# Kernel tuning notes

Measured on AMD Instinct MI355X. Metric: run time of the kernel, lower is better.

## Reference

```python
import jax, jax.numpy as jnp
import numpy as np

N_NODES = 100000
N_EDGES = 1600000
IN_CH = 128
HID = 128
BN_EPS = 1e-5


def setup_inputs() -> dict:
    key = jax.random.key(0)
    ks = jax.random.split(key, 16)
    x = jax.random.normal(ks[0], (N_NODES, IN_CH), dtype=jnp.float32)
    edge_index = jax.random.randint(ks[1], (2, N_EDGES), 0, N_NODES, dtype=jnp.int32)
    edge_attr = jax.random.uniform(ks[2], (N_EDGES,), dtype=jnp.float32)
    def glorot(k, fan_in, fan_out):
        s = jnp.sqrt(6.0 / (fan_in + fan_out))
        return jax.random.uniform(k, (fan_in, fan_out), dtype=jnp.float32, minval=-s, maxval=s)
    W1 = glorot(ks[3], IN_CH, HID)
    b1 = jnp.zeros((HID,), jnp.float32)
    gamma1 = jnp.ones((HID,), jnp.float32)
    beta1 = jnp.zeros((HID,), jnp.float32)
    W2 = glorot(ks[4], HID, HID)
    b2 = jnp.zeros((HID,), jnp.float32)
    gamma2 = jnp.ones((HID,), jnp.float32)
    beta2 = jnp.zeros((HID,), jnp.float32)
    W3 = glorot(ks[5], HID, 1)
    b3 = jnp.zeros((1,), jnp.float32)
    return {"x": x, "edge_index": edge_index, "edge_attr": edge_attr,
            "W1": W1, "b1": b1, "gamma1": gamma1, "beta1": beta1,
            "W2": W2, "b2": b2, "gamma2": gamma2, "beta2": beta2,
            "W3": W3, "b3": b3}


def _gcn_norm(edge_index, edge_weight, num_nodes):
    # PyG gcn_norm with add_self_loops=True, self-loop weight 1.0
    sl = jnp.arange(num_nodes, dtype=edge_index.dtype)
    row = jnp.concatenate([edge_index[0], sl])  # source
    col = jnp.concatenate([edge_index[1], sl])  # target
    w = jnp.concatenate([edge_weight, jnp.ones((num_nodes,), edge_weight.dtype)])
    deg = jax.ops.segment_sum(w, col, num_segments=num_nodes)
    dinv = jnp.where(deg > 0, jax.lax.rsqrt(jnp.maximum(deg, 1e-30)), 0.0)
    norm = dinv[row] * w * dinv[col]
    return row, col, norm


def _gcn_conv(x, W, b, row, col, norm, num_nodes):
    xw = x @ W                       # [N, out]
    msg = xw[row] * norm[:, None]    # gather + scale, [E+N, out]
    out = jax.ops.segment_sum(msg, col, num_segments=num_nodes)  # scatter-add
    return out + b


def _batchnorm(x, gamma, beta):
    mean = jnp.mean(x, axis=0)
    var = jnp.mean(jnp.square(x - mean), axis=0)  # biased var (torch BN)
    return (x - mean) * jax.lax.rsqrt(var + BN_EPS) * gamma + beta


def reference(x, edge_index, edge_attr, W1, b1, gamma1, beta1, W2, b2, gamma2, beta2, W3, b3):
    n = x.shape[0]
    row, col, norm = _gcn_norm(edge_index, edge_attr, n)
    h = _gcn_conv(x, W1, b1, row, col, norm, n)
    h = jax.nn.relu(_batchnorm(h, gamma1, beta1))  # dropout = identity (eval)
    h = _gcn_conv(h, W2, b2, row, col, norm, n)
    h = jax.nn.relu(_batchnorm(h, gamma2, beta2))
    out = _gcn_conv(h, W3, b3, row, col, norm, n)  # [N, 1]
    return out
```

## Files before the change

kernel.cpp:

```cpp
#include <hip/hip_runtime.h>
#include <hip/hip_bf16.h>


#define HID 128
#define BN_EPS 1e-5f
#define BK 64

typedef __attribute__((ext_vector_type(8))) short bf16x8;
typedef __attribute__((ext_vector_type(4))) float f32x4;

static inline size_t alignup(size_t x){ return (x + 255) & ~(size_t)255; }


__global__ void k_initcur(int* cursor, int n){
  int i = blockIdx.x*256 + threadIdx.x;
  if (i < n) cursor[i] = 0;
}

__global__ void k_fill_direct(const int* __restrict__ ei, const float* __restrict__ attr,
                              int* __restrict__ cursor, int2* __restrict__ csr, int E){
  int e = blockIdx.x*256 + threadIdx.x;
  if (e >= E) return;
  int src = ei[e];
  int dst = ei[E + e];
  int pos = atomicAdd(&cursor[dst], 1);
  if (pos < BK)
    csr[(size_t)dst*BK + pos] = make_int2(src, __float_as_int(attr[e]));
}

__global__ __launch_bounds__(256) void k_degdinv(const int2* __restrict__ csr,
    const int* __restrict__ cursor, float* __restrict__ dinv, int N){
  int node = blockIdx.x*32 + (threadIdx.x >> 3);
  int l = threadIdx.x & 7;
  if (node >= N) return;
  int m = min(cursor[node], BK);
  float s = 0.f;
  for (int j = l; j < m; j += 8)
    s += __int_as_float(csr[(size_t)node*BK + j].y);
  s += __shfl_xor(s, 1, 8);
  s += __shfl_xor(s, 2, 8);
  s += __shfl_xor(s, 4, 8);
  if (l == 0) dinv[node] = 1.0f / sqrtf(1.0f + s);
}

__global__ __launch_bounds__(256) void k_wfin(int2* __restrict__ csr,
    const int* __restrict__ cursor, const float* __restrict__ dinv, int N){
  int node = blockIdx.x*32 + (threadIdx.x >> 3);
  int l = threadIdx.x & 7;
  if (node >= N) return;
  int m = min(cursor[node], BK);
  float di = dinv[node];
  for (int j = l; j < m; j += 8){
    int2 t = csr[(size_t)node*BK + j];
    float w = dinv[t.x] * __int_as_float(t.y) * di;
    csr[(size_t)node*BK + j] = make_int2(t.x, __float_as_int(w));
  }
}


static __device__ inline float2 bf16pair(unsigned int u){
  __hip_bfloat162 h = *(__hip_bfloat162*)&u;
  return __bfloat1622float2(h);
}

static __device__ inline unsigned int packpair(float x, float y){
  __hip_bfloat162 p = __float22bfloat162_rn({x, y});
  return *(unsigned int*)&p;
}

static __device__ inline uint2 pack_bf16x4(float4 a){
  uint2 r;
  r.x = packpair(a.x, a.y);
  r.y = packpair(a.z, a.w);
  return r;
}

static __device__ inline unsigned short bfbits(float v){
  __hip_bfloat16 h = __float2bfloat16(v);
  return *(unsigned short*)&h;
}

__global__ void k_wtprep(const float* __restrict__ Wg, unsigned short* __restrict__ WTg){
  int idx = blockIdx.x*256 + threadIdx.x;
  int k   = idx >> 7;
  int col = idx & 127;
  WTg[(size_t)col*128 + k] = bfbits(Wg[(size_t)k*128 + col]);
}

template<bool BN, bool AB16>
__device__ inline void gemm_body(const void* __restrict__ Av,
    const unsigned short* __restrict__ WTg, const float* __restrict__ coef,
    unsigned int* __restrict__ C, int n, int bid){
  int lane = threadIdx.x & 63;
  int wv4  = threadIdx.x >> 6;
  int l16  = lane & 15;
  int kg   = lane >> 4;
  int row_base = bid*128 + wv4*32;
  int nm1 = n - 1;
  int a0row = min(row_base + l16,      nm1);
  int a1row = min(row_base + 16 + l16, nm1);

  f32x4 acc[2][8] = {};
  #pragma unroll
  for (int k0 = 0; k0 < 128; k0 += 32){
    int k = k0 + kg*8;
    float4 sca, scb, sha, shb;
    if (BN){
      sca = *(const float4*)(coef + k);
      scb = *(const float4*)(coef + k + 4);
      sha = *(const float4*)(coef + 128 + k);
      shb = *(const float4*)(coef + 128 + k + 4);
    }
    bf16x8 a0, a1;
    if constexpr (AB16){
      const unsigned int* A = (const unsigned int*)Av;
      uint4 u0 = *(const uint4*)(A + (size_t)a0row*64 + (k >> 1));
      uint4 u1 = *(const uint4*)(A + (size_t)a1row*64 + (k >> 1));
      #pragma unroll
      for (int half = 0; half < 2; ++half){
        uint4 u = half ? u1 : u0;
        float2 p0 = bf16pair(u.x), p1 = bf16pair(u.y);
        float2 p2 = bf16pair(u.z), p3 = bf16pair(u.w);
        if (BN){
          p0.x = fmaxf(fmaf(p0.x, sca.x, sha.x), 0.f);
          p0.y = fmaxf(fmaf(p0.y, sca.y, sha.y), 0.f);
          p1.x = fmaxf(fmaf(p1.x, sca.z, sha.z), 0.f);
          p1.y = fmaxf(fmaf(p1.y, sca.w, sha.w), 0.f);
          p2.x = fmaxf(fmaf(p2.x, scb.x, shb.x), 0.f);
          p2.y = fmaxf(fmaf(p2.y, scb.y, shb.y), 0.f);
          p3.x = fmaxf(fmaf(p3.x, scb.z, shb.z), 0.f);
          p3.y = fmaxf(fmaf(p3.y, scb.w, shb.w), 0.f);
        }
        union { bf16x8 v; unsigned int u[4]; } c;
        c.u[0] = packpair(p0.x, p0.y);
        c.u[1] = packpair(p1.x, p1.y);
        c.u[2] = packpair(p2.x, p2.y);
        c.u[3] = packpair(p3.x, p3.y);
        if (half) a1 = c.v; else a0 = c.v;
      }
    } else {
      const float* A = (const float*)Av;
      float4 lo0 = *(const float4*)(A + (size_t)a0row*HID + k);
      float4 hi0 = *(const float4*)(A + (size_t)a0row*HID + k + 4);
      float4 lo1 = *(const float4*)(A + (size_t)a1row*HID + k);
      float4 hi1 = *(const float4*)(A + (size_t)a1row*HID + k + 4);
      union { bf16x8 v; uint2 u[2]; } a0c, a1c;
      a0c.u[0] = pack_bf16x4(lo0); a0c.u[1] = pack_bf16x4(hi0);
      a1c.u[0] = pack_bf16x4(lo1); a1c.u[1] = pack_bf16x4(hi1);
      a0 = a0c.v; a1 = a1c.v;
    }
    #pragma unroll
    for (int ct = 0; ct < 8; ++ct){
      int col = ct*16 + l16;
      bf16x8 b = *(const bf16x8*)(WTg + (size_t)col*128 + k);
      acc[0][ct] = __builtin_amdgcn_mfma_f32_16x16x32_bf16(a0, b, acc[0][ct], 0,0,0);
      acc[1][ct] = __builtin_amdgcn_mfma_f32_16x16x32_bf16(a1, b, acc[1][ct], 0,0,0);
    }
  }

  #pragma unroll
  for (int rt = 0; rt < 2; ++rt){
    int growb = row_base + rt*16 + kg*4;
    #pragma unroll
    for (int ct = 0; ct < 8; ++ct){
      #pragma unroll
      for (int r = 0; r < 4; ++r){
        float v = acc[rt][ct][r];
        float o = __shfl_xor(v, 1);
        if (!(lane & 1)){
          int grow = growb + r;
          if (grow < n){
            C[(size_t)grow*64 + ct*8 + (l16 >> 1)] = packpair(v, o);
          }
        }
      }
    }
  }
}

__global__ __launch_bounds__(256) void k_gemm_mfma(const float* __restrict__ A,
    const unsigned short* __restrict__ WTg,
    unsigned int* __restrict__ C, int n){
  gemm_body<false,false>(A, WTg, nullptr, C, n, blockIdx.x);
}

__global__ __launch_bounds__(256) void k_gemm_mfma_bn16(const unsigned int* __restrict__ A,
    const unsigned short* __restrict__ WTg, const float* __restrict__ coef,
    unsigned int* __restrict__ C, int n){
  gemm_body<true,true>(A, WTg, coef, C, n, blockIdx.x);
}


struct Acc8 { float a0,a1,a2,a3,a4,a5,a6,a7; };

static __device__ inline void fma8(Acc8& a, uint4 v, float wt){
  float2 p0 = bf16pair(v.x), p1 = bf16pair(v.y);
  float2 p2 = bf16pair(v.z), p3 = bf16pair(v.w);
  a.a0 = fmaf(wt, p0.x, a.a0); a.a1 = fmaf(wt, p0.y, a.a1);
  a.a2 = fmaf(wt, p1.x, a.a2); a.a3 = fmaf(wt, p1.y, a.a3);
  a.a4 = fmaf(wt, p2.x, a.a4); a.a5 = fmaf(wt, p2.y, a.a5);
  a.a6 = fmaf(wt, p3.x, a.a6); a.a7 = fmaf(wt, p3.y, a.a7);
}

__global__ __launch_bounds__(256) void k_gather128(const unsigned int* __restrict__ xwb,
    const int2* __restrict__ csr, const int* __restrict__ cursor,
    const float* __restrict__ dinv, const float* __restrict__ bias,
    unsigned int* __restrict__ out, int n){
  int node = blockIdx.x*4 + (threadIdx.x >> 6);
  int lane = threadIdx.x & 63;
  if (node >= n) return;
  int l16 = lane & 15;
  int eg  = lane >> 4;
  size_t base = (size_t)node*BK;
  int m = min(cursor[node], BK);
  Acc8 a = {0,0,0,0,0,0,0,0};
  if (eg == 0){
    float di = dinv[node];
    float sw = di * di;
    uint4 sv = *(const uint4*)(xwb + (size_t)node*64 + l16*4);
    float4 b0 = *(const float4*)(bias + l16*8);
    float4 b1 = *(const float4*)(bias + l16*8 + 4);
    a.a0 = b0.x; a.a1 = b0.y; a.a2 = b0.z; a.a3 = b0.w;
    a.a4 = b1.x; a.a5 = b1.y; a.a6 = b1.z; a.a7 = b1.w;
    fma8(a, sv, sw);
  }
  int j = eg;
  for (; j + 12 < m; j += 16){
    int2 e0 = csr[base + j];
    int2 e1 = csr[base + j + 4];
    int2 e2 = csr[base + j + 8];
    int2 e3 = csr[base + j + 12];
    uint4 v0 = *(const uint4*)(xwb + (size_t)e0.x*64 + l16*4);
    uint4 v1 = *(const uint4*)(xwb + (size_t)e1.x*64 + l16*4);
    uint4 v2 = *(const uint4*)(xwb + (size_t)e2.x*64 + l16*4);
    uint4 v3 = *(const uint4*)(xwb + (size_t)e3.x*64 + l16*4);
    fma8(a, v0, __int_as_float(e0.y));
    fma8(a, v1, __int_as_float(e1.y));
    fma8(a, v2, __int_as_float(e2.y));
    fma8(a, v3, __int_as_float(e3.y));
  }
  for (; j < m; j += 4){
    int2 ea = csr[base + j];
    uint4 va = *(const uint4*)(xwb + (size_t)ea.x*64 + l16*4);
    fma8(a, va, __int_as_float(ea.y));
  }
  a.a0 += __shfl_xor(a.a0, 16); a.a1 += __shfl_xor(a.a1, 16);
  a.a2 += __shfl_xor(a.a2, 16); a.a3 += __shfl_xor(a.a3, 16);
  a.a4 += __shfl_xor(a.a4, 16); a.a5 += __shfl_xor(a.a5, 16);
  a.a6 += __shfl_xor(a.a6, 16); a.a7 += __shfl_xor(a.a7, 16);
  a.a0 += __shfl_xor(a.a0, 32); a.a1 += __shfl_xor(a.a1, 32);
  a.a2 += __shfl_xor(a.a2, 32); a.a3 += __shfl_xor(a.a3, 32);
  a.a4 += __shfl_xor(a.a4, 32); a.a5 += __shfl_xor(a.a5, 32);
  a.a6 += __shfl_xor(a.a6, 32); a.a7 += __shfl_xor(a.a7, 32);
  if (eg == 0){
    uint4 r;
    r.x = packpair(a.a0, a.a1);
    r.y = packpair(a.a2, a.a3);
    r.z = packpair(a.a4, a.a5);
    r.w = packpair(a.a6, a.a7);
    *(uint4*)(out + (size_t)node*64 + l16*4) = r;
  }
}

__global__ __launch_bounds__(256) void k_bnstats(const unsigned int* __restrict__ h,
                                                 float* stats, int n){
  __shared__ float ls0[256], ls1[256], lq0[256], lq1[256];
  int p  = threadIdx.x & 63;
  int r0 = blockIdx.x*4 + (threadIdx.x >> 6);
  float s0=0.f, s1=0.f, q0=0.f, q1=0.f;
  for (int r = r0; r < n; r += gridDim.x*4){
    float2 v = bf16pair(h[(size_t)r*64 + p]);
    s0 += v.x; q0 = fmaf(v.x, v.x, q0);
    s1 += v.y; q1 = fmaf(v.y, v.y, q1);
  }
  ls0[threadIdx.x]=s0; ls1[threadIdx.x]=s1; lq0[threadIdx.x]=q0; lq1[threadIdx.x]=q1;
  __syncthreads();
  if (threadIdx.x < 64){
    int t = threadIdx.x;
    s0 = ls0[t]+ls0[t+64]+ls0[t+128]+ls0[t+192];
    s1 = ls1[t]+ls1[t+64]+ls1[t+128]+ls1[t+192];
    q0 = lq0[t]+lq0[t+64]+lq0[t+128]+lq0[t+192];
    q1 = lq1[t]+lq1[t+64]+lq1[t+128]+lq1[t+192];
    atomicAdd(&stats[2*t],       s0);
    atomicAdd(&stats[2*t+1],     s1);
    atomicAdd(&stats[128+2*t],   q0);
    atomicAdd(&stats[128+2*t+1], q1);
  }
}

__global__ void k_bnfin(const float* __restrict__ stats, const float* __restrict__ gamma,
                        const float* __restrict__ beta, float* coef, int n){
  int c = threadIdx.x;
  float inv_n = 1.0f / (float)n;
  float mean = stats[c] * inv_n;
  float var = fmaxf(stats[128 + c] * inv_n - mean*mean, 0.f);
  float sc = gamma[c] / sqrtf(var + BN_EPS);
  coef[c] = sc;
  coef[128 + c] = fmaf(-mean, sc, beta[c]);
}

__global__ __launch_bounds__(256) void k_dotW3(const unsigned int* __restrict__ h,
    const float* __restrict__ coef, const float* __restrict__ W3,
    float* __restrict__ xw3, int n){
  int lane = threadIdx.x & 31;
  int row = blockIdx.x*8 + (threadIdx.x >> 5);
  if (row >= n) return;
  uint2 u = *(const uint2*)(h + (size_t)row*64 + lane*2);
  float2 va = bf16pair(u.x), vb = bf16pair(u.y);
  float4 sc = *(const float4*)(coef + lane*4);
  float4 sh = *(const float4*)(coef + 128 + lane*4);
  float4 w  = *(const float4*)(W3 + lane*4);
  float acc = fmaxf(fmaf(va.x, sc.x, sh.x), 0.f) * w.x
            + fmaxf(fmaf(va.y, sc.y, sh.y), 0.f) * w.y
            + fmaxf(fmaf(vb.x, sc.z, sh.z), 0.f) * w.z
            + fmaxf(fmaf(vb.y, sc.w, sh.w), 0.f) * w.w;
  #pragma unroll
  for (int mm = 1; mm < 32; mm <<= 1) acc += __shfl_xor(acc, mm, 32);
  if (lane == 0) xw3[row] = acc;
}

__global__ void k_gather1(const float* __restrict__ xw3, const int2* __restrict__ csr,
    const int* __restrict__ cursor, const float* __restrict__ dinv,
    const float* __restrict__ b3, float* __restrict__ out, int n){
  int i = blockIdx.x*256 + threadIdx.x;
  if (i >= n) return;
  float di = dinv[i];
  float acc = fmaf(di*di, xw3[i], b3[0]);
  size_t base = (size_t)i*BK;
  int m = min(cursor[i], BK);
  for (int j = 0; j < m; ++j){
    int2 e = csr[base + j];
    acc = fmaf(__int_as_float(e.y), xw3[e.x], acc);
  }
  out[i] = acc;
}

extern "C" void kernel_launch(void* const* d_in, const int* in_sizes, int n_in,
                              void* d_out, int out_size, void* d_ws, size_t ws_size,
                              hipStream_t stream){
  const float* x    = (const float*)d_in[0];
  const int*   ei   = (const int*)  d_in[1];
  const float* attr = (const float*)d_in[2];
  const float* W1   = (const float*)d_in[3];
  const float* b1   = (const float*)d_in[4];
  const float* g1   = (const float*)d_in[5];
  const float* be1  = (const float*)d_in[6];
  const float* W2   = (const float*)d_in[7];
  const float* b2   = (const float*)d_in[8];
  const float* g2   = (const float*)d_in[9];
  const float* be2  = (const float*)d_in[10];
  const float* W3   = (const float*)d_in[11];
  const float* b3   = (const float*)d_in[12];
  float* out = (float*)d_out;

  const int N = in_sizes[0] / HID;
  const int E = in_sizes[2];

  char* w = (char*)d_ws;
  auto take = [&](size_t bytes) -> char* { char* p = w; w += alignup(bytes); return p; };
  int*   cursor = (int*)  take((size_t)N*4);
  float* dinv   = (float*)take((size_t)N*4);
  float* stats  = (float*)take(256*4);
  float* coef1  = (float*)take(256*4);
  float* coef2  = (float*)take(256*4);
  unsigned short* wt1 = (unsigned short*)take(128*128*2);
  unsigned short* wt2 = (unsigned short*)take(128*128*2);
  int2*  csr    = (int2*) take((size_t)N*BK*8);
  float* xw3    = (float*)take((size_t)N*4);
  unsigned int* bufA = (unsigned int*)take((size_t)N*64*4);
  unsigned int* bufB = (unsigned int*)take((size_t)N*64*4);
  (void)ws_size; (void)n_in; (void)out_size;

  int nbN = (N + 255)/256;
  int nbE = (E + 255)/256;
  int nbG = (N + 127)/128;
  int nb8 = (N + 31)/32;

  k_initcur    <<<nbN, 256, 0, stream>>>(cursor, N);
  k_wtprep     <<<64,  256, 0, stream>>>(W1, wt1);
  k_wtprep     <<<64,  256, 0, stream>>>(W2, wt2);
  k_fill_direct<<<nbE, 256, 0, stream>>>(ei, attr, cursor, csr, E);
  k_gemm_mfma  <<<nbG, 256, 0, stream>>>(x, wt1, bufA, N);
  k_degdinv    <<<nb8, 256, 0, stream>>>(csr, cursor, dinv, N);
  k_wfin       <<<nb8, 256, 0, stream>>>(csr, cursor, dinv, N);

  k_gather128  <<<(N+3)/4, 256, 0, stream>>>(bufA, csr, cursor, dinv, b1, bufB, N);
  hipMemsetAsync(stats, 0, 256*4, stream);
  k_bnstats    <<<512, 256, 0, stream>>>(bufB, stats, N);
  k_bnfin      <<<1, 128, 0, stream>>>(stats, g1, be1, coef1, N);

  k_gemm_mfma_bn16<<<nbG, 256, 0, stream>>>(bufB, wt2, coef1, bufA, N);
  k_gather128  <<<(N+3)/4, 256, 0, stream>>>(bufA, csr, cursor, dinv, b2, bufB, N);
  hipMemsetAsync(stats, 0, 256*4, stream);
  k_bnstats    <<<512, 256, 0, stream>>>(bufB, stats, N);
  k_bnfin      <<<1, 128, 0, stream>>>(stats, g2, be2, coef2, N);

  k_dotW3      <<<(N+7)/8, 256, 0, stream>>>(bufB, coef2, W3, xw3, N);
  k_gather1    <<<nbN, 256, 0, stream>>>(xw3, csr, cursor, dinv, b3, out, N);
}
```

Before: 447.9 us.

## Split CSR fill atomics into 8 sub-cursors per node with compaction pass

Edge fill now spreads atomics across 8 per-node sub-counters chosen by block index, with each sub-bucket holding up to 8 slots. A compaction kernel then prefix-scans the sub-counts to pack the entries and compute degree sums, and a single-block pass inserts overflow edges. The aim is to cut same-address atomic contention during CSR construction. In exchange it adds an 8N counter memset, extra CSR read/write traffic, and a serial overflow kernel. Overflow beyond the fixed capacity is silently dropped, and the order of neighbours changes.

Measured after the change: 485.4 us. 1.08x slower.

```diff
diff --git a/kernel.cpp b/kernel.cpp
--- a/kernel.cpp
+++ b/kernel.cpp
@@ -5,6 +5,8 @@
 #define HID 128
 #define BN_EPS 1e-5f
 #define BK 64
+#define SUBK 8
+#define OVF_CAP 8192
 
 typedef __attribute__((ext_vector_type(8))) short bf16x8;
 typedef __attribute__((ext_vector_type(4))) float f32x4;
@@ -12,43 +14,84 @@
 static inline size_t alignup(size_t x){ return (x + 255) & ~(size_t)255; }
 
 
-__global__ void k_initcur(int* cursor, int n){
-  int i = blockIdx.x*256 + threadIdx.x;
-  if (i < n) cursor[i] = 0;
-}
-
-__global__ void k_fill_direct(const int* __restrict__ ei, const float* __restrict__ attr,
-                              int* __restrict__ cursor, int2* __restrict__ csr, int E){
+__global__ void k_fill_sub(const int* __restrict__ ei, const float* __restrict__ attr,
+                           int* __restrict__ curR, int2* __restrict__ csr,
+                           int* __restrict__ ovf_cnt, int4* __restrict__ ovf,
+                           int N, int E){
   int e = blockIdx.x*256 + threadIdx.x;
   if (e >= E) return;
+  int r = blockIdx.x & 7;
   int src = ei[e];
   int dst = ei[E + e];
-  int pos = atomicAdd(&cursor[dst], 1);
-  if (pos < BK)
-    csr[(size_t)dst*BK + pos] = make_int2(src, __float_as_int(attr[e]));
-}
-
-__global__ __launch_bounds__(256) void k_degdinv(const int2* __restrict__ csr,
-    const int* __restrict__ cursor, float* __restrict__ dinv, int N){
+  int ab = __float_as_int(attr[e]);
+  int pos = atomicAdd(&curR[(size_t)r*N + dst], 1);
+  if (pos < SUBK){
+    csr[(size_t)dst*BK + r*SUBK + pos] = make_int2(src, ab);
+  } else {
+    int oi = atomicAdd(ovf_cnt, 1);
+    if (oi < OVF_CAP) ovf[oi] = make_int4(src, dst, ab, 0);
+  }
+}
+
+__global__ __launch_bounds__(256) void k_compact(int2* __restrict__ csr,
+    const int* __restrict__ curR, int* __restrict__ cnt,
+    float* __restrict__ degsum, int N){
   int node = blockIdx.x*32 + (threadIdx.x >> 3);
   int l = threadIdx.x & 7;
   if (node >= N) return;
-  int m = min(cursor[node], BK);
+  int c = min(curR[(size_t)l*N + node], SUBK);
+  size_t base = (size_t)node*BK;
+  int2 e[SUBK];
+  #pragma unroll
+  for (int k = 0; k < SUBK; ++k)
+    e[k] = csr[base + l*SUBK + k];
+  int incl = c;
+  #pragma unroll
+  for (int d = 1; d < 8; d <<= 1){
+    int t = __shfl_up(incl, d, 8);
+    if (l >= d) incl += t;
+  }
+  int o = incl - c;
   float s = 0.f;
-  for (int j = l; j < m; j += 8)
-    s += __int_as_float(csr[(size_t)node*BK + j].y);
+  for (int k = 0; k < c; ++k){
+    csr[base + o + k] = e[k];
+    s += __int_as_float(e[k].y);
+  }
   s += __shfl_xor(s, 1, 8);
   s += __shfl_xor(s, 2, 8);
   s += __shfl_xor(s, 4, 8);
-  if (l == 0) dinv[node] = 1.0f / sqrtf(1.0f + s);
+  int total = __shfl(incl, 7, 8);
+  if (l == 0){
+    cnt[node] = total;
+    degsum[node] = s;
+  }
+}
+
+__global__ void k_ovf(const int* __restrict__ ovf_cnt, const int4* __restrict__ ovf,
+                      int2* __restrict__ csr, int* __restrict__ cnt,
+                      float* __restrict__ degsum){
+  int n = min(*ovf_cnt, OVF_CAP);
+  for (int i = threadIdx.x; i < n; i += 256){
+    int4 t = ovf[i];
+    int pos = atomicAdd(&cnt[t.y], 1);
+    if (pos < BK){
+      csr[(size_t)t.y*BK + pos] = make_int2(t.x, t.z);
+      atomicAdd(&degsum[t.y], __int_as_float(t.z));
+    }
+  }
+}
+
+__global__ void k_dinv(const float* __restrict__ degsum, float* __restrict__ dinv, int N){
+  int i = blockIdx.x*256 + threadIdx.x;
+  if (i < N) dinv[i] = 1.0f / sqrtf(1.0f + degsum[i]);
 }
 
 __global__ __launch_bounds__(256) void k_wfin(int2* __restrict__ csr,
-    const int* __restrict__ cursor, const float* __restrict__ dinv, int N){
+    const int* __restrict__ cnt, const float* __restrict__ dinv, int N){
   int node = blockIdx.x*32 + (threadIdx.x >> 3);
   int l = threadIdx.x & 7;
   if (node >= N) return;
-  int m = min(cursor[node], BK);
+  int m = min(cnt[node], BK);
   float di = dinv[node];
   for (int j = l; j < m; j += 8){
     int2 t = csr[(size_t)node*BK + j];
@@ -203,7 +246,7 @@
 }
 
 __global__ __launch_bounds__(256) void k_gather128(const unsigned int* __restrict__ xwb,
-    const int2* __restrict__ csr, const int* __restrict__ cursor,
+    const int2* __restrict__ csr, const int* __restrict__ cnt,
     const float* __restrict__ dinv, const float* __restrict__ bias,
     unsigned int* __restrict__ out, int n){
   int node = blockIdx.x*4 + (threadIdx.x >> 6);
@@ -212,7 +255,7 @@
   int l16 = lane & 15;
   int eg  = lane >> 4;
   size_t base = (size_t)node*BK;
-  int m = min(cursor[node], BK);
+  int m = min(cnt[node], BK);
   Acc8 a = {0,0,0,0,0,0,0,0};
   if (eg == 0){
     float di = dinv[node];
@@ -320,14 +363,14 @@
 }
 
 __global__ void k_gather1(const float* __restrict__ xw3, const int2* __restrict__ csr,
-    const int* __restrict__ cursor, const float* __restrict__ dinv,
+    const int* __restrict__ cnt, const float* __restrict__ dinv,
     const float* __restrict__ b3, float* __restrict__ out, int n){
   int i = blockIdx.x*256 + threadIdx.x;
   if (i >= n) return;
   float di = dinv[i];
   float acc = fmaf(di*di, xw3[i], b3[0]);
   size_t base = (size_t)i*BK;
-  int m = min(cursor[i], BK);
+  int m = min(cnt[i], BK);
   for (int j = 0; j < m; ++j){
     int2 e = csr[base + j];
     acc = fmaf(__int_as_float(e.y), xw3[e.x], acc);
@@ -358,8 +401,12 @@
 
   char* w = (char*)d_ws;
   auto take = [&](size_t bytes) -> char* { char* p = w; w += alignup(bytes); return p; };
-  int*   cursor = (int*)  take((size_t)N*4);
+  int*   curR   = (int*)  take((size_t)8*N*4);
+  int*   cnt    = (int*)  take((size_t)N*4);
+  float* degsum = (float*)take((size_t)N*4);
   float* dinv   = (float*)take((size_t)N*4);
+  int*   ovfcnt = (int*)  take(256);
+  int4*  ovf    = (int4*) take((size_t)OVF_CAP*16);
   float* stats  = (float*)take(256*4);
   float* coef1  = (float*)take(256*4);
   float* coef2  = (float*)take(256*4);
@@ -376,25 +423,28 @@
   int nbG = (N + 127)/128;
   int nb8 = (N + 31)/32;
 
-  k_initcur    <<<nbN, 256, 0, stream>>>(cursor, N);
-  k_wtprep     <<<64,  256, 0, stream>>>(W1, wt1);
-  k_wtprep     <<<64,  256, 0, stream>>>(W2, wt2);
-  k_fill_direct<<<nbE, 256, 0, stream>>>(ei, attr, cursor, csr, E);
-  k_gemm_mfma  <<<nbG, 256, 0, stream>>>(x, wt1, bufA, N);
-  k_degdinv    <<<nb8, 256, 0, stream>>>(csr, cursor, dinv, N);
-  k_wfin       <<<nb8, 256, 0, stream>>>(csr, cursor, dinv, N);
-
-  k_gather128  <<<(N+3)/4, 256, 0, stream>>>(bufA, csr, cursor, dinv, b1, bufB, N);
+  hipMemsetAsync(curR, 0, (size_t)8*N*4, stream);
+  hipMemsetAsync(ovfcnt, 0, 4, stream);
+  k_wtprep   <<<64,  256, 0, stream>>>(W1, wt1);
+  k_wtprep   <<<64,  256, 0, stream>>>(W2, wt2);
+  k_fill_sub <<<nbE, 256, 0, stream>>>(ei, attr, curR, csr, ovfcnt, ovf, N, E);
+  k_gemm_mfma<<<nbG, 256, 0, stream>>>(x, wt1, bufA, N);
+  k_compact  <<<nb8, 256, 0, stream>>>(csr, curR, cnt, degsum, N);
+  k_ovf      <<<1,   256, 0, stream>>>(ovfcnt, ovf, csr, cnt, degsum);
+  k_dinv     <<<nbN, 256, 0, stream>>>(degsum, dinv, N);
+  k_wfin     <<<nb8, 256, 0, stream>>>(csr, cnt, dinv, N);
+
+  k_gather128<<<(N+3)/4, 256, 0, stream>>>(bufA, csr, cnt, dinv, b1, bufB, N);
   hipMemsetAsync(stats, 0, 256*4, stream);
-  k_bnstats    <<<512, 256, 0, stream>>>(bufB, stats, N);
-  k_bnfin      <<<1, 128, 0, stream>>>(stats, g1, be1, coef1, N);
+  k_bnstats  <<<512, 256, 0, stream>>>(bufB, stats, N);
+  k_bnfin    <<<1, 128, 0, stream>>>(stats, g1, be1, coef1, N);
 
   k_gemm_mfma_bn16<<<nbG, 256, 0, stream>>>(bufB, wt2, coef1, bufA, N);
-  k_gather128  <<<(N+3)/4, 256, 0, stream>>>(bufA, csr, cursor, dinv, b2, bufB, N);
+  k_gather128<<<(N+3)/4, 256, 0, stream>>>(bufA, csr, cnt, dinv, b2, bufB, N);
   hipMemsetAsync(stats, 0, 256*4, stream);
-  k_bnstats    <<<512, 256, 0, stream>>>(bufB, stats, N);
-  k_bnfin      <<<1, 128, 0, stream>>>(stats, g2, be2, coef2, N);
-
-  k_dotW3      <<<(N+7)/8, 256, 0, stream>>>(bufB, coef2, W3, xw3, N);
-  k_gather1    <<<nbN, 256, 0, stream>>>(xw3, csr, cursor, dinv, b3, out, N);
-}
+  k_bnstats  <<<512, 256, 0, stream>>>(bufB, stats, N);
+  k_bnfin    <<<1, 128, 0, stream>>>(stats, g2, be2, coef2, N);
+
+  k_dotW3    <<<(N+7)/8, 256, 0, stream>>>(bufB, coef2, W3, xw3, N);
+  k_gather1  <<<nbN, 256, 0, stream>>>(xw3, csr, cnt, dinv, b3, out, N);
+}
```
